# Kernel tuning notes

Hardware: AMD Instinct MI355X
Metric: run time of the kernel (lower is better)

## Reference

```python
import jax, jax.numpy as jnp
import numpy as np

N_CLUSTERS = 1024
EMBED_DIM = 256
BETA = 0.25
EPS = 1e-05


def setup_inputs() -> dict:
    key = jax.random.key(0)
    k1, k2 = jax.random.split(key)
    z = jax.random.normal(k1, (16, 64, 64, EMBED_DIM), dtype=jnp.float32)
    # nn.init.uniform_(codebook, -1/K, 1/K)
    bound = 1.0 / N_CLUSTERS
    codebook = jax.random.uniform(k2, (N_CLUSTERS, EMBED_DIM), dtype=jnp.float32,
                                  minval=-bound, maxval=bound)
    return {"z": z, "codebook": codebook}


def reference(z, codebook):
    K = codebook.shape[0]
    # squared distances: ||z||^2 + ||e||^2 - 2 z.e  -> [B,V,P,K]
    z2 = jnp.sum(z * z, axis=-1, keepdims=True)          # [B,V,P,1]
    e2 = jnp.sum(codebook * codebook, axis=-1)           # [K]
    ze = jnp.einsum('bvpd,kd->bvpk', z, codebook)        # [B,V,P,K]
    dist = z2 + e2[None, None, None, :] - 2.0 * ze
    indices = jnp.argmin(dist, axis=-1)                  # [B,V,P] int
    z_q = codebook[indices]                              # gather [B,V,P,D]
    z_q_st = z + jax.lax.stop_gradient(z_q - z)          # straight-through

    codebook_loss = jnp.mean((z_q - jax.lax.stop_gradient(z)) ** 2)
    commitment_loss = jnp.mean((z - jax.lax.stop_gradient(z_q)) ** 2)
    cluster_loss = codebook_loss + BETA * commitment_loss

    # perplexity stats (no grad)
    counts = jnp.zeros((K,), dtype=jnp.float32).at[indices.ravel()].add(1.0)
    probs = counts / (counts.sum() + EPS)
    perplexity = jnp.exp(-jnp.sum(probs * jnp.log(probs + EPS)))

    return z_q_st, commitment_loss, codebook_loss, cluster_loss, perplexity, indices
```

## Files before the change

### kernel.cpp

```cpp
#include <hip/hip_runtime.h>
#include <cfloat>
#include <math.h>

#define P_TOT 65536
#define DIM   256
#define KTOT  1024
#define BETA_ 0.25f
#define EPS_  1e-5f
#define MARGIN_ 1.5e-4f

#define OUT_LOSS_OFF ((size_t)P_TOT * DIM)
#define OUT_IDX_OFF  (OUT_LOSS_OFF + 4)

typedef __attribute__((ext_vector_type(8))) short s16x8;
typedef __attribute__((ext_vector_type(4))) float f32x4;

__device__ __forceinline__ unsigned short f2bf(float x) {
    unsigned u = __float_as_uint(x);
    u += 0x7FFFu + ((u >> 16) & 1u);
    return (unsigned short)(u >> 16);
}
__device__ __forceinline__ float bf2f(unsigned short h) {
    return __uint_as_float(((unsigned)h) << 16);
}
__device__ __forceinline__ void gl16(const void* g, void* l) {
    __builtin_amdgcn_global_load_lds(
        (const __attribute__((address_space(1))) unsigned int*)g,
        (__attribute__((address_space(3))) unsigned int*)l, 16, 0, 0);
}

__global__ __launch_bounds__(256) void vq_pre(
    const float* __restrict__ z, const float* __restrict__ cb,
    float* __restrict__ z2, float* __restrict__ e2,
    unsigned short* __restrict__ cbh, unsigned short* __restrict__ cbl,
    unsigned int* __restrict__ hist,
    float* __restrict__ loss_sum, unsigned int* __restrict__ flag_cnt,
    float* __restrict__ out)
{
    const int tid = threadIdx.x;
    const int lane = tid & 63;
    const int wave = tid >> 6;
    const int bid = blockIdx.x;

    if (bid < P_TOT / 4) {
        const int p = bid * 4 + wave;
        float4 v = *(const float4*)(z + (size_t)p * DIM + lane * 4);
        float s = v.x * v.x + v.y * v.y + v.z * v.z + v.w * v.w;
        #pragma unroll
        for (int off = 32; off > 0; off >>= 1) s += __shfl_down(s, off, 64);
        if (lane == 0) z2[p] = s;

        unsigned short h0 = f2bf(v.x), h1 = f2bf(v.y), h2 = f2bf(v.z), h3 = f2bf(v.w);
        unsigned short l0 = f2bf(v.x - bf2f(h0)), l1 = f2bf(v.y - bf2f(h1));
        unsigned short l2 = f2bf(v.z - bf2f(h2)), l3 = f2bf(v.w - bf2f(h3));
        uint2 hp, lp;
        hp.x = (unsigned)h0 | ((unsigned)h1 << 16); hp.y = (unsigned)h2 | ((unsigned)h3 << 16);
        lp.x = (unsigned)l0 | ((unsigned)l1 << 16); lp.y = (unsigned)l2 | ((unsigned)l3 << 16);
        char* rowb = (char*)out + (size_t)p * 1024;
        *(uint2*)(rowb + lane * 8) = hp;
        *(uint2*)(rowb + 512 + lane * 8) = lp;
    } else {
        const int rel = bid - P_TOT / 4;
        const int k = rel * 4 + wave;
        float4 v = *(const float4*)(cb + (size_t)k * DIM + lane * 4);
        float s = v.x * v.x + v.y * v.y + v.z * v.z + v.w * v.w;
        #pragma unroll
        for (int off = 32; off > 0; off >>= 1) s += __shfl_down(s, off, 64);
        if (lane == 0) e2[k] = s;

        unsigned short h0 = f2bf(v.x), h1 = f2bf(v.y), h2 = f2bf(v.z), h3 = f2bf(v.w);
        unsigned short l0 = f2bf(v.x - bf2f(h0)), l1 = f2bf(v.y - bf2f(h1));
        unsigned short l2 = f2bf(v.z - bf2f(h2)), l3 = f2bf(v.w - bf2f(h3));
        uint2 hp, lp;
        hp.x = (unsigned)h0 | ((unsigned)h1 << 16); hp.y = (unsigned)h2 | ((unsigned)h3 << 16);
        lp.x = (unsigned)l0 | ((unsigned)l1 << 16); lp.y = (unsigned)l2 | ((unsigned)l3 << 16);
        *(uint2*)(cbh + (size_t)k * DIM + lane * 4) = hp;
        *(uint2*)(cbl + (size_t)k * DIM + lane * 4) = lp;

        if (rel < 4) hist[rel * 256 + tid] = 0u;
        if (rel == 4 && tid == 0) { *loss_sum = 0.0f; *flag_cnt = 0u; }
    }
}

#define BM 128
#define BN 128

__global__ __launch_bounds__(256, 2) void vq_argmin(
    const float* __restrict__ z, const float* __restrict__ cb,
    const unsigned short* __restrict__ cbh, const unsigned short* __restrict__ cbl,
    const float* __restrict__ z2, const float* __restrict__ e2,
    unsigned int* __restrict__ hist, float* __restrict__ loss_sum,
    unsigned int* __restrict__ flag_cnt, unsigned int* __restrict__ flag_list,
    float* __restrict__ out)
{
    __shared__ __align__(16) char sm[65536];
    __shared__ int kwin[BM];
    __shared__ unsigned char flgs[BM];
    __shared__ float wred[4];

    const int tid = threadIdx.x;
    const int lane = tid & 63;
    const int wid = tid >> 6;
    const int wm = wid >> 1, wn = wid & 1;
    const int col = lane & 15;
    const int lg  = lane >> 4;
    const int swz = lane & 7;
    const int row0 = blockIdx.x * BM;

    const char* zsB  = (const char*)out;
    const char* cbhB = (const char*)cbh;
    const char* cblB = (const char*)cbl;

    float b1[16], b2[16]; int i1[16];
    float z2r[16];
    #pragma unroll
    for (int q = 0; q < 16; ++q) {
        b1[q] = FLT_MAX; b2[q] = FLT_MAX; i1[q] = 0;
        z2r[q] = z2[row0 + wm * 64 + (q >> 2) * 16 + lg * 4 + (q & 3)];
    }

    int aRow[4], bRow[4];
    #pragma unroll
    for (int f = 0; f < 4; ++f) {
        aRow[f] = (wm * 64 + f * 16 + col) * 128;
        bRow[f] = (wn * 64 + f * 16 + col) * 128;
    }
    const int bc0 = ((0 + lg) ^ swz) << 4;
    const int bc1 = ((4 + lg) ^ swz) << 4;

    const int sr  = lane >> 3;
    const int scb = lane & 7;

    #pragma unroll 1
    for (int nc = 0; nc < KTOT / BN; ++nc) {
        const int n0 = nc * BN;
        f32x4 acc[4][4];
        #pragma unroll
        for (int fm = 0; fm < 4; ++fm)
            #pragma unroll
            for (int fn = 0; fn < 4; ++fn)
                acc[fm][fn] = (f32x4){0.0f, 0.0f, 0.0f, 0.0f};

        #pragma unroll 1
        for (int kc = 0; kc < 4; ++kc) {
            __syncthreads();
            #pragma unroll
            for (int i = 0; i < 4; ++i) {
                const int rloc = wid * 32 + i * 8 + sr;
                const int cb16 = ((scb ^ (rloc & 7)) << 4);
                const size_t aoff = ((size_t)(row0 + rloc) << 10) + (kc << 7);
                const size_t boff = ((size_t)(n0 + rloc) << 9) + (kc << 7);
                char* lb = sm + (wid * 32 + i * 8) * 128;
                gl16(zsB + aoff + cb16,        lb);
                gl16(zsB + aoff + 512 + cb16,  lb + 16384);
                gl16(cbhB + boff + cb16,       lb + 32768);
                gl16(cblB + boff + cb16,       lb + 49152);
            }
            __syncthreads();
            #pragma unroll
            for (int ks = 0; ks < 2; ++ks) {
                const int bc = ks ? bc1 : bc0;
                s16x8 ah[4], al[4], bh[4], bl[4];
                #pragma unroll
                for (int f = 0; f < 4; ++f) {
                    ah[f] = *(const s16x8*)(sm + aRow[f] + bc);
                    al[f] = *(const s16x8*)(sm + 16384 + aRow[f] + bc);
                    bh[f] = *(const s16x8*)(sm + 32768 + bRow[f] + bc);
                    bl[f] = *(const s16x8*)(sm + 49152 + bRow[f] + bc);
                }
                #pragma unroll
                for (int fm = 0; fm < 4; ++fm)
                    #pragma unroll
                    for (int fn = 0; fn < 4; ++fn) {
                        acc[fm][fn] = __builtin_amdgcn_mfma_f32_16x16x32_bf16(
                            ah[fm], bh[fn], acc[fm][fn], 0, 0, 0);
                        acc[fm][fn] = __builtin_amdgcn_mfma_f32_16x16x32_bf16(
                            ah[fm], bl[fn], acc[fm][fn], 0, 0, 0);
                        acc[fm][fn] = __builtin_amdgcn_mfma_f32_16x16x32_bf16(
                            al[fm], bh[fn], acc[fm][fn], 0, 0, 0);
                    }
            }
        }
        float e2v[4];
        #pragma unroll
        for (int fn = 0; fn < 4; ++fn) e2v[fn] = e2[n0 + wn * 64 + fn * 16 + col];
        #pragma unroll
        for (int fm = 0; fm < 4; ++fm)
            #pragma unroll
            for (int fn = 0; fn < 4; ++fn)
                #pragma unroll
                for (int r4 = 0; r4 < 4; ++r4) {
                    const int q = fm * 4 + r4;
                    const float dist = (z2r[q] + e2v[fn]) - 2.0f * acc[fm][fn][r4];
                    const int idx = n0 + wn * 64 + fn * 16 + col;
                    if (dist < b1[q]) { b2[q] = b1[q]; b1[q] = dist; i1[q] = idx; }
                    else if (dist < b2[q]) { b2[q] = dist; }
                }
    }

    __syncthreads();
    float* Rb1 = (float*)sm;
    float* Rb2 = (float*)(sm + 16896);
    int*   Ri1 = (int*)(sm + 33792);
    const int slot = col + 16 * wn;
    #pragma unroll
    for (int q = 0; q < 16; ++q) {
        const int px = wm * 64 + (q >> 2) * 16 + lg * 4 + (q & 3);
        Rb1[px * 33 + slot] = b1[q];
        Rb2[px * 33 + slot] = b2[q];
        Ri1[px * 33 + slot] = i1[q];
    }
    __syncthreads();
    if (tid < BM) {
        float x1 = Rb1[tid * 33], x2 = Rb2[tid * 33]; int xi = Ri1[tid * 33];
        for (int s = 1; s < 32; ++s) {
            const float c1 = Rb1[tid * 33 + s], c2 = Rb2[tid * 33 + s];
            const int ci = Ri1[tid * 33 + s];
            const float nb2 = fminf(fmaxf(x1, c1), fminf(x2, c2));
            if (c1 < x1 || (c1 == x1 && ci < xi)) { x1 = c1; xi = ci; }
            x2 = nb2;
        }
        kwin[tid] = xi;
        const bool fl = (x2 - x1) <= MARGIN_;
        flgs[tid] = fl ? 1 : 0;
        if (fl) {
            const unsigned pos = atomicAdd(flag_cnt, 1u);
            flag_list[pos] = (unsigned)(row0 + tid);
        } else {
            out[OUT_IDX_OFF + row0 + tid] = (float)xi;
            atomicAdd(&hist[xi], 1u);
        }
    }
    __syncthreads();

    float lacc = 0.0f;
    #pragma unroll 4
    for (int i = 0; i < 32; ++i) {
        const int flat4 = tid + i * 256;
        const int row = flat4 >> 6;
        if (!flgs[row]) {
            const int dj = (flat4 & 63) * 4;
            const size_t zoff = (size_t)(row0 + row) * DIM + dj;
            float4 zv = *(const float4*)(z + zoff);
            float4 ev = *(const float4*)(cb + (size_t)kwin[row] * DIM + dj);
            float dx = ev.x - zv.x, dy = ev.y - zv.y, dz = ev.z - zv.z, dw = ev.w - zv.w;
            float4 o;
            o.x = zv.x + dx; o.y = zv.y + dy; o.z = zv.z + dz; o.w = zv.w + dw;
            *(float4*)(out + zoff) = o;
            lacc += dx * dx + dy * dy + dz * dz + dw * dw;
        }
    }
    #pragma unroll
    for (int off = 32; off > 0; off >>= 1) lacc += __shfl_down(lacc, off, 64);
    if (lane == 0) wred[wid] = lacc;
    __syncthreads();
    if (tid == 0) atomicAdd(loss_sum, wred[0] + wred[1] + wred[2] + wred[3]);
}

__global__ __launch_bounds__(256) void vq_fix(
    const float* __restrict__ z, const float* __restrict__ cb,
    const float* __restrict__ z2, const float* __restrict__ e2,
    const unsigned int* __restrict__ flag_cnt, const unsigned int* __restrict__ flag_list,
    unsigned int* __restrict__ hist, float* __restrict__ loss_sum,
    float* __restrict__ out)
{
    __shared__ float zrow[4][DIM];
    __shared__ float zz2[4];
    __shared__ int pxid[4];
    __shared__ float rb[4][256];
    __shared__ int   ri[4][256];
    __shared__ int   kw4[4];

    const int tid = threadIdx.x;
    const int total = (int)*flag_cnt;

    for (int base = blockIdx.x * 4; base < total; base += gridDim.x * 4) {
        const int npx = min(4, total - base);
        __syncthreads();
        if (tid < 4) {
            const int p = (int)flag_list[base + (tid < npx ? tid : 0)];
            pxid[tid] = p; zz2[tid] = z2[p];
        }
        __syncthreads();
        {
            const int q = tid >> 6, d = (tid & 63) * 4;
            float4 v = *(const float4*)(z + (size_t)pxid[q] * DIM + d);
            *(float4*)&zrow[q][d] = v;
        }
        __syncthreads();

        const int k0 = tid * 4;
        float acc[4][4];
        #pragma unroll
        for (int q = 0; q < 4; ++q)
            #pragma unroll
            for (int j = 0; j < 4; ++j) acc[q][j] = 0.0f;

        for (int d4 = 0; d4 < 64; ++d4) {
            float4 cv[4];
            #pragma unroll
            for (int j = 0; j < 4; ++j)
                cv[j] = *(const float4*)(cb + (size_t)(k0 + j) * DIM + d4 * 4);
            #pragma unroll
            for (int q = 0; q < 4; ++q) {
                float4 zv = *(const float4*)&zrow[q][d4 * 4];
                #pragma unroll
                for (int j = 0; j < 4; ++j) {
                    acc[q][j] = fmaf(zv.x, cv[j].x, acc[q][j]);
                    acc[q][j] = fmaf(zv.y, cv[j].y, acc[q][j]);
                    acc[q][j] = fmaf(zv.z, cv[j].z, acc[q][j]);
                    acc[q][j] = fmaf(zv.w, cv[j].w, acc[q][j]);
                }
            }
        }
        #pragma unroll
        for (int q = 0; q < 4; ++q) {
            float bd = FLT_MAX; int bi = 0;
            #pragma unroll
            for (int j = 0; j < 4; ++j) {
                const int k = k0 + j;
                const float dist = (zz2[q] + e2[k]) - 2.0f * acc[q][j];
                if (dist < bd) { bd = dist; bi = k; }
            }
            rb[q][tid] = bd; ri[q][tid] = bi;
        }
        __syncthreads();
        {
            const int q = tid >> 6, lane = tid & 63;
            float bd = rb[q][lane]; int bi = ri[q][lane];
            #pragma unroll
            for (int s = 1; s < 4; ++s) {
                const float d2 = rb[q][lane + s * 64]; const int i2 = ri[q][lane + s * 64];
                if (d2 < bd || (d2 == bd && i2 < bi)) { bd = d2; bi = i2; }
            }
            #pragma unroll
            for (int off = 32; off > 0; off >>= 1) {
                const float d2 = __shfl_down(bd, off, 64);
                const int i2 = __shfl_down(bi, off, 64);
                if (d2 < bd || (d2 == bd && i2 < bi)) { bd = d2; bi = i2; }
            }
            if (lane == 0) kw4[q] = bi;
        }
        __syncthreads();
        {
            const int q = tid >> 6, lane = tid & 63;
            if (q < npx) {
                const int p = pxid[q];
                const int kw = kw4[q];
                const int d = lane * 4;
                float4 zv = *(const float4*)&zrow[q][d];
                float4 ev = *(const float4*)(cb + (size_t)kw * DIM + d);
                float dx = ev.x - zv.x, dy = ev.y - zv.y, dz = ev.z - zv.z, dw = ev.w - zv.w;
                float4 o;
                o.x = zv.x + dx; o.y = zv.y + dy; o.z = zv.z + dz; o.w = zv.w + dw;
                *(float4*)(out + (size_t)p * DIM + d) = o;
                float lacc = dx * dx + dy * dy + dz * dz + dw * dw;
                #pragma unroll
                for (int off = 32; off > 0; off >>= 1) lacc += __shfl_down(lacc, off, 64);
                if (lane == 0) {
                    atomicAdd(loss_sum, lacc);
                    out[OUT_IDX_OFF + p] = (float)kw;
                    atomicAdd(&hist[kw], 1u);
                }
            }
        }
    }
}

__global__ __launch_bounds__(1024) void vq_finalize(
    const unsigned int* __restrict__ hist, const float* __restrict__ loss_sum,
    float* __restrict__ out)
{
    __shared__ float sred[16];
    __shared__ float totalsh;
    const int tid = threadIdx.x;
    const float c = (float)hist[tid];

    float t = c;
    #pragma unroll
    for (int off = 32; off > 0; off >>= 1) t += __shfl_down(t, off, 64);
    if ((tid & 63) == 0) sred[tid >> 6] = t;
    __syncthreads();
    if (tid == 0) {
        float s = 0.0f;
        for (int i = 0; i < 16; ++i) s += sred[i];
        totalsh = s;
    }
    __syncthreads();
    const float total = totalsh;
    const float prob = c / (total + EPS_);
    float term = prob * logf(prob + EPS_);
    __syncthreads();
    #pragma unroll
    for (int off = 32; off > 0; off >>= 1) term += __shfl_down(term, off, 64);
    if ((tid & 63) == 0) sred[tid >> 6] = term;
    __syncthreads();
    if (tid == 0) {
        float s = 0.0f;
        for (int i = 0; i < 16; ++i) s += sred[i];
        const float perp = expf(-s);
        const float S = *loss_sum;
        const float mean = S / (float)(P_TOT * DIM);
        out[OUT_LOSS_OFF + 0] = mean;
        out[OUT_LOSS_OFF + 1] = mean;
        out[OUT_LOSS_OFF + 2] = mean + BETA_ * mean;
        out[OUT_LOSS_OFF + 3] = perp;
    }
}

extern "C" void kernel_launch(void* const* d_in, const int* in_sizes, int n_in,
                              void* d_out, int out_size, void* d_ws, size_t ws_size,
                              hipStream_t stream) {
    const float* z  = (const float*)d_in[0];
    const float* cb = (const float*)d_in[1];
    float* out = (float*)d_out;

    float* z2 = (float*)d_ws;
    float* e2 = z2 + P_TOT;
    unsigned int* hist = (unsigned int*)(e2 + KTOT);
    float* loss_sum = (float*)(hist + KTOT);
    unsigned int* flag_cnt = (unsigned int*)(loss_sum + 1);
    unsigned int* flag_list = flag_cnt + 1;
    unsigned short* cbh = (unsigned short*)(((uintptr_t)(flag_list + P_TOT) + 15) & ~(uintptr_t)15);
    unsigned short* cbl = cbh + (size_t)KTOT * DIM;

    vq_pre<<<P_TOT / 4 + KTOT / 4, 256, 0, stream>>>(z, cb, z2, e2, cbh, cbl,
                                                     hist, loss_sum, flag_cnt, out);
    vq_argmin<<<P_TOT / BM, 256, 0, stream>>>(z, cb, cbh, cbl, z2, e2,
                                              hist, loss_sum, flag_cnt, flag_list, out);
    vq_fix<<<1024, 256, 0, stream>>>(z, cb, z2, e2, flag_cnt, flag_list,
                                     hist, loss_sum, out);
    vq_finalize<<<1, 1024, 0, stream>>>(hist, loss_sum, out);
}
```

Baseline: 387.6 us.

## Raise MFMA wave priority and process eight pixels per fix-up block

```diff
diff --git a/kernel.cpp b/kernel.cpp
--- a/kernel.cpp
+++ b/kernel.cpp
@@ -168,6 +168,7 @@
                     bh[f] = *(const s16x8*)(sm + 32768 + bRow[f] + bc);
                     bl[f] = *(const s16x8*)(sm + 49152 + bRow[f] + bc);
                 }
+                __builtin_amdgcn_s_setprio(1);
                 #pragma unroll
                 for (int fm = 0; fm < 4; ++fm)
                     #pragma unroll
@@ -179,6 +180,7 @@
                         acc[fm][fn] = __builtin_amdgcn_mfma_f32_16x16x32_bf16(
                             al[fm], bh[fn], acc[fm][fn], 0, 0, 0);
                     }
+                __builtin_amdgcn_s_setprio(0);
             }
         }
         float e2v[4];
@@ -257,6 +259,7 @@
     if (tid == 0) atomicAdd(loss_sum, wred[0] + wred[1] + wred[2] + wred[3]);
 }
 
+#define FPX 8
 __global__ __launch_bounds__(256) void vq_fix(
     const float* __restrict__ z, const float* __restrict__ cb,
     const float* __restrict__ z2, const float* __restrict__ e2,
@@ -264,35 +267,38 @@
     unsigned int* __restrict__ hist, float* __restrict__ loss_sum,
     float* __restrict__ out)
 {
-    __shared__ float zrow[4][DIM];
-    __shared__ float zz2[4];
-    __shared__ int pxid[4];
-    __shared__ float rb[4][256];
-    __shared__ int   ri[4][256];
-    __shared__ int   kw4[4];
+    __shared__ float zrow[FPX][DIM];
+    __shared__ float zz2[FPX];
+    __shared__ int pxid[FPX];
+    __shared__ float rb[FPX][256];
+    __shared__ int   ri[FPX][256];
+    __shared__ int   kw8[FPX];
 
     const int tid = threadIdx.x;
+    const int wave = tid >> 6;
+    const int lane = tid & 63;
     const int total = (int)*flag_cnt;
 
-    for (int base = blockIdx.x * 4; base < total; base += gridDim.x * 4) {
-        const int npx = min(4, total - base);
+    for (int base = blockIdx.x * FPX; base < total; base += gridDim.x * FPX) {
+        const int npx = min(FPX, total - base);
         __syncthreads();
-        if (tid < 4) {
+        if (tid < FPX) {
             const int p = (int)flag_list[base + (tid < npx ? tid : 0)];
             pxid[tid] = p; zz2[tid] = z2[p];
         }
         __syncthreads();
-        {
-            const int q = tid >> 6, d = (tid & 63) * 4;
-            float4 v = *(const float4*)(z + (size_t)pxid[q] * DIM + d);
-            *(float4*)&zrow[q][d] = v;
+        #pragma unroll
+        for (int r = wave; r < FPX; r += 4) {
+            const int d = lane * 4;
+            float4 v = *(const float4*)(z + (size_t)pxid[r] * DIM + d);
+            *(float4*)&zrow[r][d] = v;
         }
         __syncthreads();
 
         const int k0 = tid * 4;
-        float acc[4][4];
-        #pragma unroll
-        for (int q = 0; q < 4; ++q)
+        float acc[FPX][4];
+        #pragma unroll
+        for (int q = 0; q < FPX; ++q)
             #pragma unroll
             for (int j = 0; j < 4; ++j) acc[q][j] = 0.0f;
 
@@ -302,7 +308,7 @@
             for (int j = 0; j < 4; ++j)
                 cv[j] = *(const float4*)(cb + (size_t)(k0 + j) * DIM + d4 * 4);
             #pragma unroll
-            for (int q = 0; q < 4; ++q) {
+            for (int q = 0; q < FPX; ++q) {
                 float4 zv = *(const float4*)&zrow[q][d4 * 4];
                 #pragma unroll
                 for (int j = 0; j < 4; ++j) {
@@ -314,7 +320,7 @@
             }
         }
         #pragma unroll
-        for (int q = 0; q < 4; ++q) {
+        for (int q = 0; q < FPX; ++q) {
             float bd = FLT_MAX; int bi = 0;
             #pragma unroll
             for (int j = 0; j < 4; ++j) {
@@ -325,12 +331,12 @@
             rb[q][tid] = bd; ri[q][tid] = bi;
         }
         __syncthreads();
-        {
-            const int q = tid >> 6, lane = tid & 63;
-            float bd = rb[q][lane]; int bi = ri[q][lane];
+        #pragma unroll
+        for (int rq = wave; rq < FPX; rq += 4) {
+            float bd = rb[rq][lane]; int bi = ri[rq][lane];
             #pragma unroll
             for (int s = 1; s < 4; ++s) {
-                const float d2 = rb[q][lane + s * 64]; const int i2 = ri[q][lane + s * 64];
+                const float d2 = rb[rq][lane + s * 64]; const int i2 = ri[rq][lane + s * 64];
                 if (d2 < bd || (d2 == bd && i2 < bi)) { bd = d2; bi = i2; }
             }
             #pragma unroll
@@ -339,16 +345,16 @@
                 const int i2 = __shfl_down(bi, off, 64);
                 if (d2 < bd || (d2 == bd && i2 < bi)) { bd = d2; bi = i2; }
             }
-            if (lane == 0) kw4[q] = bi;
+            if (lane == 0) kw8[rq] = bi;
         }
         __syncthreads();
-        {
-            const int q = tid >> 6, lane = tid & 63;
-            if (q < npx) {
-                const int p = pxid[q];
-                const int kw = kw4[q];
+        #pragma unroll
+        for (int rq = wave; rq < FPX; rq += 4) {
+            if (rq < npx) {
+                const int p = pxid[rq];
+                const int kw = kw8[rq];
                 const int d = lane * 4;
-                float4 zv = *(const float4*)&zrow[q][d];
+                float4 zv = *(const float4*)&zrow[rq][d];
                 float4 ev = *(const float4*)(cb + (size_t)kw * DIM + d);
                 float dx = ev.x - zv.x, dy = ev.y - zv.y, dz = ev.z - zv.z, dw = ev.w - zv.w;
                 float4 o;
```

Result: faster. 340.5 us (-12.2%).
